# Performance work log

Measured on AMD Instinct MI355X. Metric: run time of the kernel, lower is better.

Reference implementation:

```python
import jax, jax.numpy as jnp
import numpy as np

B, T, C = 2, 2048, 1024
H = 16
D = C // H  # head_dim = 64


def setup_inputs() -> dict:
    key = jax.random.key(0)
    k1, k2, k3, k4 = jax.random.split(key, 4)
    x = jax.random.normal(k1, (B, T, C), dtype=jnp.float32)
    # parameter scales ~ torch default init magnitude
    w_qkv = jax.random.normal(k2, (C, 3 * C), dtype=jnp.float32) * (1.0 / np.sqrt(C))
    w_proj = jax.random.normal(k3, (C, C), dtype=jnp.float32) * (1.0 / np.sqrt(C))
    b_proj = jax.random.normal(k4, (C,), dtype=jnp.float32) * 0.01
    return {"x": x, "w_qkv": w_qkv, "w_proj": w_proj, "b_proj": b_proj}


def reference(x, w_qkv, w_proj, b_proj):
    b, t, c = x.shape
    scale = 1.0 / jnp.sqrt(jnp.asarray(D, dtype=x.dtype))
    qkv = x @ w_qkv                                   # [B,T,3C]
    q, k, v = jnp.split(qkv, 3, axis=-1)
    def heads(u):  # [B,T,C] -> [B,H,T,D]
        return u.reshape(b, t, H, D).transpose(0, 2, 1, 3)
    q, k, v = heads(q), heads(k), heads(v)
    attn = jnp.einsum('bhqd,bhkd->bhqk', q, k) * scale  # [B,H,T,T]
    causal = jnp.tril(jnp.ones((t, t), dtype=bool))
    attn = jnp.where(causal, attn, -jnp.inf)
    attn = jax.nn.softmax(attn, axis=-1)
    # dropout p=0.0 / eval mode: identity
    out = jnp.einsum('bhqk,bhkd->bhqd', attn, v)        # [B,H,T,D]
    out = out.transpose(0, 2, 1, 3).reshape(b, t, c)
    return out @ w_proj + b_proj
```

## Files before the change

kernel.cpp:

```cpp
#include <hip/hip_runtime.h>
#include <stdint.h>

#define Bn 2
#define Tn 2048
#define Cn 1024
#define Hn 16
#define Dn 64
#define Mn (Bn*Tn)

typedef __attribute__((ext_vector_type(8))) short bf16x8;
typedef __attribute__((ext_vector_type(4))) float f32x4;
typedef __attribute__((ext_vector_type(4))) unsigned int u32x4;
typedef __attribute__((ext_vector_type(2))) unsigned int u32x2;
typedef unsigned short u16;

__device__ __forceinline__ u16 f2bf(float f) {
  union { float f; uint32_t u; } v; v.f = f;
  uint32_t u = v.u;
  return (u16)((u + 0x7fffu + ((u >> 16) & 1u)) >> 16);
}

__device__ __forceinline__ uint32_t pk_bf16(float lo, float hi) {
  uint32_t r;
  asm volatile("v_cvt_pk_bf16_f32 %0, %1, %2" : "=v"(r) : "v"(lo), "v"(hi));
  return r;
}

__device__ __forceinline__ void async16(const void* g, void* lds) {
  __builtin_amdgcn_global_load_lds((const __attribute__((address_space(1))) void*)g,
                                   (__attribute__((address_space(3))) void*)lds,
                                   16, 0, 0);
}


__global__ void cvt_x(const float* __restrict__ x, u16* __restrict__ xb) {
  int i = (blockIdx.x * 256 + threadIdx.x) * 4;
  float4 v = *(const float4*)(x + i);
  ushort4 o;
  o.x = f2bf(v.x); o.y = f2bf(v.y); o.z = f2bf(v.z); o.w = f2bf(v.w);
  *(ushort4*)(xb + i) = o;
}

template<int K, int N>
__global__ void cvt_T(const float* __restrict__ in, u16* __restrict__ out) {
  __shared__ float tile[32][33];
  int n0 = blockIdx.x * 32, k0 = blockIdx.y * 32;
  int tx = threadIdx.x & 31, ty = threadIdx.x >> 5;
  #pragma unroll
  for (int i = 0; i < 32; i += 8)
    tile[ty + i][tx] = in[(size_t)(k0 + ty + i) * N + n0 + tx];
  __syncthreads();
  #pragma unroll
  for (int i = 0; i < 32; i += 8)
    out[(size_t)(n0 + ty + i) * K + k0 + tx] = f2bf(tile[tx][ty + i]);
}


template<int EPI>
__launch_bounds__(256, 3)
__global__ void gemm_bt(const u16* __restrict__ A, const u16* __restrict__ Bt, int N,
                        u16* __restrict__ Qb, u16* __restrict__ Kb, u16* __restrict__ Vb,
                        float* __restrict__ Out, const float* __restrict__ bias) {
  constexpr int Kd = 1024;
  __shared__ u16 As[128][64];
  __shared__ u16 Bs[128][64];
  const int nT = N >> 7;
  const int cpx = gridDim.x >> 3;
  const int wg = (blockIdx.x & 7) * cpx + (blockIdx.x >> 3);
  const int m0 = (wg / nT) << 7;
  const int n0 = (wg % nT) << 7;
  const int tid = threadIdx.x;
  const int lane = tid & 63, wid = tid >> 6;
  const int wr = wid >> 1, wc = wid & 1;
  const int lr = lane & 15, lg = lane >> 4;

  f32x4 acc[4][4] = {};

  for (int kb = 0; kb < Kd; kb += 64) {
    #pragma unroll
    for (int i = 0; i < 4; ++i) {
      int c = (wid * 4 + i) * 64 + lane;
      int row = c >> 3, ko = (c & 7) << 3;
      async16(A + (size_t)(m0 + row) * Kd + kb + ko, &As[0][0] + c * 8);
      async16(Bt + (size_t)(n0 + row) * Kd + kb + ko, &Bs[0][0] + c * 8);
    }
    __syncthreads();
    bf16x8 af[2][4], bf[2][4];
    #pragma unroll
    for (int kc = 0; kc < 2; ++kc) {
      #pragma unroll
      for (int mi = 0; mi < 4; ++mi) {
        af[kc][mi] = *(const bf16x8*)&As[wr * 64 + mi * 16 + lr][kc * 32 + lg * 8];
        bf[kc][mi] = *(const bf16x8*)&Bs[wc * 64 + mi * 16 + lr][kc * 32 + lg * 8];
      }
    }
    #pragma unroll
    for (int kc = 0; kc < 2; ++kc)
      #pragma unroll
      for (int mi = 0; mi < 4; ++mi)
        #pragma unroll
        for (int ni = 0; ni < 4; ++ni)
          acc[mi][ni] = __builtin_amdgcn_mfma_f32_16x16x32_bf16(af[kc][mi], bf[kc][ni], acc[mi][ni], 0, 0, 0);
    __syncthreads();
  }

  if constexpr (EPI == 0) {
    #pragma unroll
    for (int mi = 0; mi < 4; ++mi) {
      int r0 = m0 + wr * 64 + mi * 16 + lg * 4;
      int bb = r0 >> 11;
      int t0 = r0 & 2047;
      #pragma unroll
      for (int ni = 0; ni < 4; ++ni) {
        int col = n0 + wc * 64 + ni * 16 + lr;
        int sel = col >> 10, rem = col & 1023;
        int h = rem >> 6, d = rem & 63;
        f32x4 v = acc[mi][ni];
        if (sel == 0) {
          size_t base = ((size_t)(bb * Hn + h) * Tn + t0) * Dn + d;
          #pragma unroll
          for (int r = 0; r < 4; ++r) Qb[base + (size_t)r * Dn] = f2bf(v[r] * 0.125f);
        } else if (sel == 1) {
          size_t base = ((size_t)(bb * Hn + h) * Tn + t0) * Dn + d;
          #pragma unroll
          for (int r = 0; r < 4; ++r) Kb[base + (size_t)r * Dn] = f2bf(v[r]);
        } else {
          size_t base = ((size_t)(bb * Hn + h) * Dn + d) * Tn + t0;
          ushort4 o;
          o.x = f2bf(v[0]); o.y = f2bf(v[1]); o.z = f2bf(v[2]); o.w = f2bf(v[3]);
          *(ushort4*)(Vb + base) = o;
        }
      }
    }
  } else {
    #pragma unroll
    for (int mi = 0; mi < 4; ++mi) {
      int r0 = m0 + wr * 64 + mi * 16 + lg * 4;
      #pragma unroll
      for (int ni = 0; ni < 4; ++ni) {
        int col = n0 + wc * 64 + ni * 16 + lr;
        float bv = bias[col];
        #pragma unroll
        for (int r = 0; r < 4; ++r)
          Out[(size_t)(r0 + r) * Cn + col] = acc[mi][ni][r] + bv;
      }
    }
  }
}


__device__ __forceinline__ void stage_kv(const u16* __restrict__ K,
                                         const u16* __restrict__ Vt, int k0,
                                         u16* __restrict__ Kbuf, u16* __restrict__ Vbuf,
                                         int tid) {
  #pragma unroll
  for (int i = 0; i < 2; ++i) {
    int c = i * 256 + tid;
    int row = c >> 3;
    int js = (c & 7) ^ (row & 7);
    async16(K + (size_t)(k0 + row) * Dn + js * 8, Kbuf + c * 8);
    async16(Vt + (size_t)row * Tn + k0 + js * 8, Vbuf + c * 8);
  }
}

__launch_bounds__(256, 3)
__global__ void attn(const u16* __restrict__ Qb, const u16* __restrict__ Kb,
                     const u16* __restrict__ Vb, u16* __restrict__ Ob) {
  __shared__ u16 __attribute__((aligned(16))) Ks[2 * 4096];
  __shared__ u16 __attribute__((aligned(16))) Vs[2 * 4096];
  __shared__ uint32_t __attribute__((aligned(16))) P32[4][16][36];

  const int raw = blockIdx.x;
  const int xcd = raw & 7;
  const int idx = raw >> 3;
  const int bh  = xcd * 4 + (idx & 3);
  const int qt  = 31 - (idx >> 2);
  const int q0  = qt * 64;
  const int nt  = qt + 1;

  const int tid = threadIdx.x;
  const int lane = tid & 63, wid = tid >> 6;
  const int lr = lane & 15, lg = lane >> 4;
  const int bb = bh >> 4, h = bh & 15;

  const u16* Q  = Qb + (size_t)bh * Tn * Dn;
  const u16* K  = Kb + (size_t)bh * Tn * Dn;
  const u16* Vt = Vb + (size_t)bh * Dn * Tn;

  const int swz = (lr & 7);
  const int qoff = wid * 16 + lr;
  const int koff0 = lg * 4;

  bf16x8 qf[2];
  qf[0] = *(const bf16x8*)(Q + (size_t)(q0 + qoff) * Dn + lg * 8);
  qf[1] = *(const bf16x8*)(Q + (size_t)(q0 + qoff) * Dn + 32 + lg * 8);

  f32x4 o[4] = {};
  float m = -1e30f, l = 0.f;

  int cur = 0;
  stage_kv(K, Vt, 0, Ks, Vs, tid);
  __syncthreads();

  for (int t = 0; t < nt; ++t) {
    if (t + 1 < nt)
      stage_kv(K, Vt, (t + 1) << 6,
               Ks + (cur ^ 1) * 4096, Vs + (cur ^ 1) * 4096, tid);

    const u16* Kc = Ks + cur * 4096;
    const u16* Vc = Vs + cur * 4096;

    f32x4 s[4] = {};
    __builtin_amdgcn_s_setprio(1);
    #pragma unroll
    for (int f = 0; f < 4; ++f) {
      const int row = f * 16 + lr;
      #pragma unroll
      for (int kc = 0; kc < 2; ++kc) {
        bf16x8 kf = *(const bf16x8*)(Kc + row * 64 + (((kc * 4 + lg) ^ swz) * 8));
        s[f] = __builtin_amdgcn_mfma_f32_16x16x32_bf16(kf, qf[kc], s[f], 0, 0, 0);
      }
    }
    __builtin_amdgcn_s_setprio(0);

    if (t == nt - 1) {
      #pragma unroll
      for (int f = 0; f < 4; ++f)
        #pragma unroll
        for (int r = 0; r < 4; ++r)
          if (f * 16 + koff0 + r > qoff) s[f][r] = -1e30f;
    }

    float pm = fmaxf(fmaxf(fmaxf(s[0][0], s[0][1]), fmaxf(s[0][2], s[0][3])),
                     fmaxf(fmaxf(s[1][0], s[1][1]), fmaxf(s[1][2], s[1][3])));
    float pm2 = fmaxf(fmaxf(fmaxf(s[2][0], s[2][1]), fmaxf(s[2][2], s[2][3])),
                      fmaxf(fmaxf(s[3][0], s[3][1]), fmaxf(s[3][2], s[3][3])));
    pm = fmaxf(pm, pm2);
    pm = fmaxf(pm, __shfl_xor(pm, 16));
    pm = fmaxf(pm, __shfl_xor(pm, 32));

    if (!__all(pm - m <= 8.f)) {
      float mn = fmaxf(m, pm);
      float fac = __expf(m - mn);
      l *= fac;
      #pragma unroll
      for (int f = 0; f < 4; ++f) {
        o[f][0] *= fac; o[f][1] *= fac; o[f][2] *= fac; o[f][3] *= fac;
      }
      m = mn;
    }

    float sum = 0.f;
    #pragma unroll
    for (int f = 0; f < 4; ++f) {
      #pragma unroll
      for (int r = 0; r < 4; ++r) {
        float p = __expf(s[f][r] - m);
        s[f][r] = p;
        sum += p;
      }
    }
    sum += __shfl_xor(sum, 16);
    sum += __shfl_xor(sum, 32);
    l += sum;

    #pragma unroll
    for (int f = 0; f < 4; ++f) {
      u32x2 w;
      w.x = pk_bf16(s[f][0], s[f][1]);
      w.y = pk_bf16(s[f][2], s[f][3]);
      *(u32x2*)&P32[wid][lr][f * 8 + lg * 2] = w;
    }

    __builtin_amdgcn_s_setprio(1);
    #pragma unroll
    for (int kc = 0; kc < 2; ++kc) {
      u32x4 p4 = *(const u32x4*)&P32[wid][lr][kc * 16 + lg * 4];
      bf16x8 pf = __builtin_bit_cast(bf16x8, p4);
      #pragma unroll
      for (int f = 0; f < 4; ++f) {
        const int row = f * 16 + lr;
        bf16x8 vf = *(const bf16x8*)(Vc + row * 64 + (((kc * 4 + lg) ^ swz) * 8));
        o[f] = __builtin_amdgcn_mfma_f32_16x16x32_bf16(vf, pf, o[f], 0, 0, 0);
      }
    }
    __builtin_amdgcn_s_setprio(0);

    __syncthreads();
    cur ^= 1;
  }

  float inv = 1.f / l;
  #pragma unroll
  for (int f = 0; f < 4; ++f) {
    u32x2 w;
    w.x = pk_bf16(o[f][0] * inv, o[f][1] * inv);
    w.y = pk_bf16(o[f][2] * inv, o[f][3] * inv);
    *(u32x2*)&P32[wid][lr][f * 8 + lg * 2] = w;
  }
  u32x4 r0 = *(const u32x4*)&P32[wid][lr][lg * 8];
  u32x4 r1 = *(const u32x4*)&P32[wid][lr][lg * 8 + 4];
  u16* obase = Ob + ((size_t)(bb * Tn + q0 + qoff)) * Cn + h * Dn + lg * 16;
  *(u32x4*)(obase) = r0;
  *(u32x4*)(obase + 8) = r1;
}


extern "C" void kernel_launch(void* const* d_in, const int* in_sizes, int n_in,
                              void* d_out, int out_size, void* d_ws, size_t ws_size,
                              hipStream_t stream) {
  const float* x = (const float*)d_in[0];
  const float* w_qkv = (const float*)d_in[1];
  const float* w_proj = (const float*)d_in[2];
  const float* b_proj = (const float*)d_in[3];
  float* out = (float*)d_out;
  char* ws = (char*)d_ws;

  u16* xb     = (u16*)(ws);
  u16* wqkvT  = (u16*)(ws + (size_t)( 8u << 20));
  u16* wprojT = (u16*)(ws + (size_t)(14u << 20));
  u16* Qb     = (u16*)(ws + (size_t)(16u << 20));
  u16* Kb     = (u16*)(ws + (size_t)(24u << 20));
  u16* Vb     = (u16*)(ws + (size_t)(32u << 20));

  cvt_x<<<dim3(4096), dim3(256), 0, stream>>>(x, xb);
  cvt_T<1024, 3072><<<dim3(96, 32), dim3(256), 0, stream>>>(w_qkv, wqkvT);
  cvt_T<1024, 1024><<<dim3(32, 32), dim3(256), 0, stream>>>(w_proj, wprojT);

  gemm_bt<0><<<dim3(32 * 24), dim3(256), 0, stream>>>(xb, wqkvT, 3072,
                                                      Qb, Kb, Vb, nullptr, nullptr);
  attn<<<dim3(1024), dim3(256), 0, stream>>>(Qb, Kb, Vb, xb );
  gemm_bt<1><<<dim3(32 * 8), dim3(256), 0, stream>>>(xb, wprojT, 1024,
                                                     nullptr, nullptr, nullptr, out, b_proj);
}
```

Measured before the change: 117.8 us.

## Use 32x32 MFMA with 128-row query tiles and register-shuffled P fragments

The attention kernel moves from 16x16x32 to 32x32x16 bf16 MFMA. Each wave now handles 32 queries, so a block covers 128 query rows and the grid halves to 512 blocks. The softmax probabilities are turned into the PV operand through lane shuffles instead of an LDS round trip, and the P32 shared buffer is removed. This is meant to raise K/V reuse per staged tile and cut LDS traffic. The costs are fewer blocks, which hurts causal load balance, more wasted masked work on the two diagonal tiles, and higher register pressure from the 16-wide accumulators.

```diff
diff --git a/kernel.cpp b/kernel.cpp
--- a/kernel.cpp
+++ b/kernel.cpp
@@ -10,6 +10,7 @@
 
 typedef __attribute__((ext_vector_type(8))) short bf16x8;
 typedef __attribute__((ext_vector_type(4))) float f32x4;
+typedef __attribute__((ext_vector_type(16))) float f32x16;
 typedef __attribute__((ext_vector_type(4))) unsigned int u32x4;
 typedef __attribute__((ext_vector_type(2))) unsigned int u32x2;
 typedef unsigned short u16;
@@ -168,41 +169,41 @@
                      const u16* __restrict__ Vb, u16* __restrict__ Ob) {
   __shared__ u16 __attribute__((aligned(16))) Ks[2 * 4096];
   __shared__ u16 __attribute__((aligned(16))) Vs[2 * 4096];
-  __shared__ uint32_t __attribute__((aligned(16))) P32[4][16][36];
 
   const int raw = blockIdx.x;
   const int xcd = raw & 7;
   const int idx = raw >> 3;
   const int bh  = xcd * 4 + (idx & 3);
-  const int qt  = 31 - (idx >> 2);
-  const int q0  = qt * 64;
-  const int nt  = qt + 1;
+  const int qt  = 15 - (idx >> 2);
+  const int q0  = qt * 128;
+  const int nt  = 2 * qt + 2;
 
   const int tid = threadIdx.x;
   const int lane = tid & 63, wid = tid >> 6;
-  const int lr = lane & 15, lg = lane >> 4;
+  const int l31 = lane & 31, hi = lane >> 5;
   const int bb = bh >> 4, h = bh & 15;
 
   const u16* Q  = Qb + (size_t)bh * Tn * Dn;
   const u16* K  = Kb + (size_t)bh * Tn * Dn;
   const u16* Vt = Vb + (size_t)bh * Dn * Tn;
 
-  const int swz = (lr & 7);
-  const int qoff = wid * 16 + lr;
-  const int koff0 = lg * 4;
-
-  bf16x8 qf[2];
-  qf[0] = *(const bf16x8*)(Q + (size_t)(q0 + qoff) * Dn + lg * 8);
-  qf[1] = *(const bf16x8*)(Q + (size_t)(q0 + qoff) * Dn + 32 + lg * 8);
-
-  f32x4 o[4] = {};
-  float m = -1e30f, l = 0.f;
+  const int swz = lane & 7;
+  const int qg = q0 + wid * 32 + l31;
+
+  bf16x8 qf[4];
+  #pragma unroll
+  for (int c = 0; c < 4; ++c)
+    qf[c] = *(const bf16x8*)(Q + (size_t)qg * Dn + c * 16 + hi * 8);
+
+  f32x16 o0 = {}, o1 = {};
+  float m = -1e30f, den = 0.f;
 
   int cur = 0;
   stage_kv(K, Vt, 0, Ks, Vs, tid);
   __syncthreads();
 
   for (int t = 0; t < nt; ++t) {
+    const int k0 = t << 6;
     if (t + 1 < nt)
       stage_kv(K, Vt, (t + 1) << 6,
                Ks + (cur ^ 1) * 4096, Vs + (cur ^ 1) * 4096, tid);
@@ -210,79 +211,73 @@
     const u16* Kc = Ks + cur * 4096;
     const u16* Vc = Vs + cur * 4096;
 
-    f32x4 s[4] = {};
+    f32x16 s0 = {}, s1 = {};
     __builtin_amdgcn_s_setprio(1);
     #pragma unroll
-    for (int f = 0; f < 4; ++f) {
-      const int row = f * 16 + lr;
-      #pragma unroll
-      for (int kc = 0; kc < 2; ++kc) {
-        bf16x8 kf = *(const bf16x8*)(Kc + row * 64 + (((kc * 4 + lg) ^ swz) * 8));
-        s[f] = __builtin_amdgcn_mfma_f32_16x16x32_bf16(kf, qf[kc], s[f], 0, 0, 0);
+    for (int c = 0; c < 4; ++c) {
+      bf16x8 kf0 = *(const bf16x8*)(Kc + l31 * 64 + (((c * 2 + hi) ^ swz) * 8));
+      bf16x8 kf1 = *(const bf16x8*)(Kc + (32 + l31) * 64 + (((c * 2 + hi) ^ swz) * 8));
+      s0 = __builtin_amdgcn_mfma_f32_32x32x16_bf16(kf0, qf[c], s0, 0, 0, 0);
+      s1 = __builtin_amdgcn_mfma_f32_32x32x16_bf16(kf1, qf[c], s1, 0, 0, 0);
+    }
+    __builtin_amdgcn_s_setprio(0);
+
+    if (t >= nt - 2) {
+      #pragma unroll
+      for (int g = 0; g < 16; ++g) {
+        int kl = (g & 3) + 8 * (g >> 2) + 4 * hi;
+        if (k0 + kl > qg)      s0[g] = -1e30f;
+        if (k0 + 32 + kl > qg) s1[g] = -1e30f;
       }
     }
-    __builtin_amdgcn_s_setprio(0);
-
-    if (t == nt - 1) {
-      #pragma unroll
-      for (int f = 0; f < 4; ++f)
-        #pragma unroll
-        for (int r = 0; r < 4; ++r)
-          if (f * 16 + koff0 + r > qoff) s[f][r] = -1e30f;
-    }
-
-    float pm = fmaxf(fmaxf(fmaxf(s[0][0], s[0][1]), fmaxf(s[0][2], s[0][3])),
-                     fmaxf(fmaxf(s[1][0], s[1][1]), fmaxf(s[1][2], s[1][3])));
-    float pm2 = fmaxf(fmaxf(fmaxf(s[2][0], s[2][1]), fmaxf(s[2][2], s[2][3])),
-                      fmaxf(fmaxf(s[3][0], s[3][1]), fmaxf(s[3][2], s[3][3])));
-    pm = fmaxf(pm, pm2);
-    pm = fmaxf(pm, __shfl_xor(pm, 16));
+
+    float pm = s0[0];
+    #pragma unroll
+    for (int g = 1; g < 16; ++g) pm = fmaxf(pm, s0[g]);
+    #pragma unroll
+    for (int g = 0; g < 16; ++g) pm = fmaxf(pm, s1[g]);
     pm = fmaxf(pm, __shfl_xor(pm, 32));
 
     if (!__all(pm - m <= 8.f)) {
       float mn = fmaxf(m, pm);
       float fac = __expf(m - mn);
-      l *= fac;
-      #pragma unroll
-      for (int f = 0; f < 4; ++f) {
-        o[f][0] *= fac; o[f][1] *= fac; o[f][2] *= fac; o[f][3] *= fac;
-      }
+      den *= fac;
+      #pragma unroll
+      for (int g = 0; g < 16; ++g) { o0[g] *= fac; o1[g] *= fac; }
       m = mn;
     }
 
     float sum = 0.f;
     #pragma unroll
-    for (int f = 0; f < 4; ++f) {
-      #pragma unroll
-      for (int r = 0; r < 4; ++r) {
-        float p = __expf(s[f][r] - m);
-        s[f][r] = p;
-        sum += p;
-      }
-    }
-    sum += __shfl_xor(sum, 16);
+    for (int g = 0; g < 16; ++g) { float p = __expf(s0[g] - m); s0[g] = p; sum += p; }
+    #pragma unroll
+    for (int g = 0; g < 16; ++g) { float p = __expf(s1[g] - m); s1[g] = p; sum += p; }
     sum += __shfl_xor(sum, 32);
-    l += sum;
-
-    #pragma unroll
-    for (int f = 0; f < 4; ++f) {
-      u32x2 w;
-      w.x = pk_bf16(s[f][0], s[f][1]);
-      w.y = pk_bf16(s[f][2], s[f][3]);
-      *(u32x2*)&P32[wid][lr][f * 8 + lg * 2] = w;
-    }
+    den += sum;
+
+    bf16x8 pfrag[4];
+    #define MKFRAG(SV, C2, OUT) { \
+      uint32_t u_ = pk_bf16(SV[8*(C2)+0], SV[8*(C2)+1]); \
+      uint32_t v_ = pk_bf16(SV[8*(C2)+2], SV[8*(C2)+3]); \
+      uint32_t w_ = pk_bf16(SV[8*(C2)+4], SV[8*(C2)+5]); \
+      uint32_t z_ = pk_bf16(SV[8*(C2)+6], SV[8*(C2)+7]); \
+      uint32_t us = __shfl_xor(u_, 32), vs = __shfl_xor(v_, 32); \
+      uint32_t ws = __shfl_xor(w_, 32), zs = __shfl_xor(z_, 32); \
+      u32x4 q4; \
+      q4.x = hi ? ws : u_; q4.y = hi ? zs : v_; \
+      q4.z = hi ? w_ : us; q4.w = hi ? z_ : vs; \
+      OUT = __builtin_bit_cast(bf16x8, q4); }
+    MKFRAG(s0, 0, pfrag[0]); MKFRAG(s0, 1, pfrag[1]);
+    MKFRAG(s1, 0, pfrag[2]); MKFRAG(s1, 1, pfrag[3]);
+    #undef MKFRAG
 
     __builtin_amdgcn_s_setprio(1);
     #pragma unroll
-    for (int kc = 0; kc < 2; ++kc) {
-      u32x4 p4 = *(const u32x4*)&P32[wid][lr][kc * 16 + lg * 4];
-      bf16x8 pf = __builtin_bit_cast(bf16x8, p4);
-      #pragma unroll
-      for (int f = 0; f < 4; ++f) {
-        const int row = f * 16 + lr;
-        bf16x8 vf = *(const bf16x8*)(Vc + row * 64 + (((kc * 4 + lg) ^ swz) * 8));
-        o[f] = __builtin_amdgcn_mfma_f32_16x16x32_bf16(vf, pf, o[f], 0, 0, 0);
-      }
+    for (int kc = 0; kc < 4; ++kc) {
+      bf16x8 vf0 = *(const bf16x8*)(Vc + l31 * 64 + (((kc * 2 + hi) ^ swz) * 8));
+      bf16x8 vf1 = *(const bf16x8*)(Vc + (32 + l31) * 64 + (((kc * 2 + hi) ^ swz) * 8));
+      o0 = __builtin_amdgcn_mfma_f32_32x32x16_bf16(vf0, pfrag[kc], o0, 0, 0, 0);
+      o1 = __builtin_amdgcn_mfma_f32_32x32x16_bf16(vf1, pfrag[kc], o1, 0, 0, 0);
     }
     __builtin_amdgcn_s_setprio(0);
 
@@ -290,19 +285,25 @@
     cur ^= 1;
   }
 
-  float inv = 1.f / l;
-  #pragma unroll
-  for (int f = 0; f < 4; ++f) {
-    u32x2 w;
-    w.x = pk_bf16(o[f][0] * inv, o[f][1] * inv);
-    w.y = pk_bf16(o[f][2] * inv, o[f][3] * inv);
-    *(u32x2*)&P32[wid][lr][f * 8 + lg * 2] = w;
-  }
-  u32x4 r0 = *(const u32x4*)&P32[wid][lr][lg * 8];
-  u32x4 r1 = *(const u32x4*)&P32[wid][lr][lg * 8 + 4];
-  u16* obase = Ob + ((size_t)(bb * Tn + q0 + qoff)) * Cn + h * Dn + lg * 16;
-  *(u32x4*)(obase) = r0;
-  *(u32x4*)(obase + 8) = r1;
+  float inv = 1.f / den;
+  uint32_t* Owv = (uint32_t*)Ks + (wid << 10);
+  #pragma unroll
+  for (int e = 0; e < 16; e += 2) {
+    uint32_t p0 = pk_bf16(o0[e] * inv, o0[e + 1] * inv);
+    uint32_t p1 = pk_bf16(o1[e] * inv, o1[e + 1] * inv);
+    int sl0 = ((e & 3) >> 1) + ((e >> 2) << 2) + (hi << 1);
+    int sl1 = sl0 + 16;
+    Owv[(l31 << 5) + (((sl0 >> 2) ^ (l31 & 7)) << 2) + (sl0 & 3)] = p0;
+    Owv[(l31 << 5) + (((sl1 >> 2) ^ (l31 & 7)) << 2) + (sl1 & 3)] = p1;
+  }
+  __syncthreads();
+  u16* obase = Ob + ((size_t)(bb * Tn + q0 + wid * 32 + l31)) * Cn + h * Dn;
+  #pragma unroll
+  for (int i = 0; i < 4; ++i) {
+    int c = (hi << 2) + i;
+    u32x4 vv = *(const u32x4*)&Owv[(l31 << 5) + ((c ^ (l31 & 7)) << 2)];
+    *(u32x4*)(obase + c * 8) = vv;
+  }
 }
 
 
@@ -329,7 +330,7 @@
 
   gemm_bt<0><<<dim3(32 * 24), dim3(256), 0, stream>>>(xb, wqkvT, 3072,
                                                       Qb, Kb, Vb, nullptr, nullptr);
-  attn<<<dim3(1024), dim3(256), 0, stream>>>(Qb, Kb, Vb, xb );
+  attn<<<dim3(512), dim3(256), 0, stream>>>(Qb, Kb, Vb, xb );
   gemm_bt<1><<<dim3(32 * 8), dim3(256), 0, stream>>>(xb, wprojT, 1024,
                                                      nullptr, nullptr, nullptr, out, b_proj);
 }
```

New measurement: 127.6 us. 1.08x slower.
